# Kernel tuning notes

Measured on AMD Instinct MI355X. Metric: run time of the kernel, lower is better.

The kernel has to match this reference:

```python
import jax, jax.numpy as jnp
import numpy as np
from jax import lax

BAD = -10000.0
K = 10
W = 512  # window_size


def setup_inputs() -> dict:
    key = jax.random.key(0)
    k1, k2, k3, k4 = jax.random.split(key, 4)
    S, B, P, D, R = 4, 256, 32768, 256, 1000
    return {
        "relation": jax.random.randint(k1, (S, B), 0, R, dtype=jnp.int32),
        "head": jax.random.randint(k2, (S, B), 0, P, dtype=jnp.int32),
        "entity_embedding": jax.random.normal(k3, (S, P, D), dtype=jnp.float32),
        "relation_embedding": jax.random.normal(k4, (R, D), dtype=jnp.float32),
    }


def reference(relation, head, entity_embedding, relation_embedding):
    S, B = relation.shape
    P, D = entity_embedding.shape[1], entity_embedding.shape[2]
    Q = S * B            # total queries after all_gather
    NBEST = K + 1
    n_rep = -(-P // W)   # ceil

    # all_gather of queries across shards (every shard sees all queries)
    rel_all = relation.reshape(-1)                                   # (Q,)
    head_emb_all = entity_embedding[jnp.arange(S)[:, None], head]    # (S,B,D)
    head_emb_all = head_emb_all.reshape(Q, D)
    # DistMult score_tails: <h, r, t> ; fold h*r into one query vector
    qvec = head_emb_all * relation_embedding[rel_all]                # (Q,D)

    init_sc = jnp.full((S, Q, NBEST), BAD, dtype=jnp.float32)
    init_ix = jnp.full((S, Q, NBEST), P, dtype=jnp.int32)

    def step(carry, w):
        sc, ix = carry
        start = w * W
        # local idx of this window, clamped like the torch mask branch
        raw = start + jnp.arange(W, dtype=jnp.int32)                 # (W,)
        valid = raw < P
        slide = jnp.where(valid, raw, P - 1)
        neg = lax.dynamic_slice_in_dim(entity_embedding,
                                       jnp.minimum(start, P - W), W, axis=1)  # (S,W,D)
        scores_w = jnp.einsum('qd,swd->sqw', qvec, neg)              # (S,Q,W)
        scores_w = scores_w + BAD * (~valid).astype(scores_w.dtype)
        all_sc = jnp.concatenate([scores_w, sc], axis=-1)            # (S,Q,W+NBEST)
        all_ix = jnp.concatenate(
            [jnp.broadcast_to(slide, (S, Q, W)), ix], axis=-1)
        top_sc, top_pos = lax.top_k(all_sc, NBEST)
        top_ix = jnp.take_along_axis(all_ix, top_pos, axis=-1)
        return (top_sc, top_ix), None

    (best_sc, best_ix), _ = lax.scan(step, (init_sc, init_ix),
                                     jnp.arange(n_rep, dtype=jnp.int32))

    # all_to_all: (src_shard, dst_shard, bs, nbest) -> (dst, src, bs, nbest)
    best_sc = best_sc.reshape(S, S, B, NBEST).transpose(1, 0, 2, 3)
    best_ix = best_ix.reshape(S, S, B, NBEST).transpose(1, 0, 2, 3)

    # mask out placeholder / padding local indices (shard_counts == P)
    best_sc = best_sc + BAD * (best_ix >= P).astype(best_sc.dtype)

    # shard_and_idx_to_entity: interleaved global ids, padded column for idx==P
    base = jnp.arange(P, dtype=jnp.int32)[None, :] * S \
        + jnp.arange(S, dtype=jnp.int32)[:, None]                    # (S,P)
    table = jnp.concatenate(
        [base, jnp.full((S, 1), -1, dtype=jnp.int32)], axis=1)       # (S,P+1)
    src = jnp.arange(S, dtype=jnp.int32)[None, :, None, None]
    best_gid = table[src, best_ix]                                   # (S,S,B,NBEST)

    # per destination shard: merge the S per-source-shard top-(k+1) lists
    sc_flat = best_sc.transpose(0, 2, 1, 3).reshape(S, B, S * NBEST)
    gid_flat = best_gid.transpose(0, 2, 1, 3).reshape(S, B, S * NBEST)
    topk_sc, topk_pos = lax.top_k(sc_flat, K)                        # (S,B,K)
    topk_gid = jnp.take_along_axis(gid_flat, topk_pos, axis=-1)
    return topk_gid, topk_sc
```

## Files before the change

kernel.cpp:

```cpp
#include <hip/hip_runtime.h>

#define SS 4
#define BB 256
#define PP 32768
#define DD 256
#define QQ 1024
#define NN 131072
#define KTOP 10
#define QTILE 128
#define NCHUNK 64
#define CHROWS 2048
#define PANEL 64
#define NPANEL (CHROWS / PANEL)
#define JCH 8
#define MSLOT 20
#define ROWG 33
#define ROWE (ROWG * 8)
#define PANB (PANEL * ROWG * 16)
#define KEYMASK 0xFFFFF800u

typedef __attribute__((ext_vector_type(8))) short bf16x8;
typedef __attribute__((ext_vector_type(4))) float f32x4;
typedef __attribute__((ext_vector_type(4))) unsigned int u32x4;

static __device__ __forceinline__ short f2bf(float f) {
    union { float f; unsigned u; } v; v.f = f;
    unsigned r = (v.u + 0x7FFFu + ((v.u >> 16) & 1u)) >> 16;
    return (short)r;
}
static __device__ __forceinline__ bf16x8 cvt8(f32x4 a, f32x4 b) {
    bf16x8 r;
    r[0] = f2bf(a[0]); r[1] = f2bf(a[1]); r[2] = f2bf(a[2]); r[3] = f2bf(a[3]);
    r[4] = f2bf(b[0]); r[5] = f2bf(b[1]); r[6] = f2bf(b[2]); r[7] = f2bf(b[3]);
    return r;
}
static __device__ __forceinline__ unsigned umax(unsigned a, unsigned b) { return a > b ? a : b; }
static __device__ __forceinline__ unsigned umin(unsigned a, unsigned b) { return a < b ? a : b; }

__global__ void convert_e_kernel(const float* __restrict__ E, short* __restrict__ Ebf) {
    size_t i = ((size_t)blockIdx.x * 256 + threadIdx.x) * 8;
    f32x4 a = *(const f32x4*)(E + i);
    f32x4 b = *(const f32x4*)(E + i + 4);
    *(bf16x8*)(Ebf + i) = cvt8(a, b);
}

__global__ void qvec_kernel(const int* __restrict__ rel, const int* __restrict__ head,
                            const float* __restrict__ E, const float* __restrict__ R,
                            short* __restrict__ qbf) {
    int q = blockIdx.x, d = threadIdx.x;
    int s1 = q >> 8;
    float f = E[((size_t)(s1 * PP + head[q])) * DD + d] * R[(size_t)rel[q] * DD + d];
    qbf[q * DD + d] = f2bf(f);
}

__launch_bounds__(512, 4)
__global__ void score_topk_kernel(const short* __restrict__ Ebf, const short* __restrict__ qbf,
                                  unsigned* __restrict__ parts) {
    __shared__ __align__(16) char smem[2 * PANB];

    const int tid  = threadIdx.x;
    const int wave = tid >> 6;
    const int lane = tid & 63;
    const int quad = lane >> 4;
    const int mrow = lane & 15;
    const int mtile = blockIdx.x >> 6;
    const int chunk = blockIdx.x & 63;

    short* buf0 = (short*)smem;
    short* buf1 = (short*)(smem + PANB);

    bf16x8 afrag[8];
    {
        const int arow = mtile * QTILE + wave * 16 + mrow;
        #pragma unroll
        for (int ks = 0; ks < 8; ks++)
            afrag[ks] = *(const bf16x8*)(qbf + arow * DD + ks * 32 + quad * 8);
    }

    unsigned lst[4][4];
    #pragma unroll
    for (int r = 0; r < 4; r++)
        #pragma unroll
        for (int i = 0; i < 4; i++) lst[r][i] = 0u;

    const int n0c = chunk * CHROWS;

    bf16x8 st[4];
    #pragma unroll
    for (int it = 0; it < 4; it++) {
        int gi = it * 512 + tid, row = gi >> 5, slot = gi & 31;
        st[it] = *(const bf16x8*)(Ebf + (size_t)(n0c + row) * DD + slot * 8);
    }
    #pragma unroll
    for (int it = 0; it < 4; it++) {
        int gi = it * 512 + tid, row = gi >> 5, slot = gi & 31;
        *(bf16x8*)(buf0 + row * ROWE + slot * 8) = st[it];
    }

    int pc = mrow;

    for (int p = 0; p < NPANEL; p++) {
        short* bp = (p & 1) ? buf1 : buf0;
        short* bn = (p & 1) ? buf0 : buf1;
        __syncthreads();
        if (p + 1 < NPANEL) {
            const int n1 = n0c + (p + 1) * PANEL;
            #pragma unroll
            for (int it = 0; it < 4; it++) {
                int gi = it * 512 + tid, row = gi >> 5, slot = gi & 31;
                st[it] = *(const bf16x8*)(Ebf + (size_t)(n1 + row) * DD + slot * 8);
            }
        }

        f32x4 acc[4];
        #pragma unroll
        for (int nt = 0; nt < 4; nt++) acc[nt] = (f32x4){0.f, 0.f, 0.f, 0.f};
        #pragma unroll
        for (int ks = 0; ks < 8; ks++) {
            #pragma unroll
            for (int nt = 0; nt < 4; nt++) {
                int brow = nt * 16 + mrow;
                bf16x8 b = *(const bf16x8*)(bp + brow * ROWE + ks * 32 + quad * 8);
                acc[nt] = __builtin_amdgcn_mfma_f32_16x16x32_bf16(afrag[ks], b, acc[nt], 0, 0, 0);
            }
        }

        #pragma unroll
        for (int nt = 0; nt < 4; nt++) {
            const unsigned coln = (unsigned)(pc + nt * 16);
            #pragma unroll
            for (int r = 0; r < 4; r++) {
                unsigned enc = __float_as_uint(acc[nt][r] + 256.0f);
                unsigned key = (enc & KEYMASK) | coln;
                unsigned n0 = umin(umax(key, lst[r][0]), lst[r][1]);
                unsigned n1 = umin(umax(key, lst[r][1]), lst[r][2]);
                unsigned n2 = umin(umax(key, lst[r][2]), lst[r][3]);
                unsigned n3 = umax(key, lst[r][3]);
                lst[r][0] = n0; lst[r][1] = n1; lst[r][2] = n2; lst[r][3] = n3;
            }
        }
        pc += 64;

        if (p + 1 < NPANEL) {
            #pragma unroll
            for (int it = 0; it < 4; it++) {
                int gi = it * 512 + tid, row = gi >> 5, slot = gi & 31;
                *(bf16x8*)(bn + row * ROWE + slot * 8) = st[it];
            }
        }
    }

    unsigned* mw = (unsigned*)(smem + wave * 4096);
    #pragma unroll
    for (int r = 0; r < 4; r++) {
        u32x4 v; v[0] = lst[r][0]; v[1] = lst[r][1]; v[2] = lst[r][2]; v[3] = lst[r][3];
        *(u32x4*)(mw + (quad * 4 + r) * 64 + mrow * 4) = v;
    }
    if (lane < 16) {
        unsigned rr[JCH];
        #pragma unroll
        for (int i = 0; i < JCH; i++) rr[i] = 0u;
        #pragma unroll
        for (int j = 0; j < 16; j++) {
            u32x4 v = *(const u32x4*)(mw + lane * 64 + j * 4);
            #pragma unroll
            for (int e = 0; e < 4; e++) {
                unsigned x = v[e];
                unsigned t0 = umin(umax(x, rr[0]), rr[1]);
                unsigned t1 = umin(umax(x, rr[1]), rr[2]);
                unsigned t2 = umin(umax(x, rr[2]), rr[3]);
                unsigned t3 = umin(umax(x, rr[3]), rr[4]);
                unsigned t4 = umin(umax(x, rr[4]), rr[5]);
                unsigned t5 = umin(umax(x, rr[5]), rr[6]);
                unsigned t6 = umin(umax(x, rr[6]), rr[7]);
                unsigned t7 = umax(x, rr[7]);
                rr[0]=t0; rr[1]=t1; rr[2]=t2; rr[3]=t3; rr[4]=t4; rr[5]=t5; rr[6]=t6; rr[7]=t7;
            }
        }
        const int qg = mtile * QTILE + wave * 16 + lane;
        unsigned* dst = parts + ((size_t)qg * NCHUNK + chunk) * JCH;
        #pragma unroll
        for (int i = 0; i < JCH; i++) dst[i] = rr[JCH - 1 - i];
    }
}

__global__ void finalize_kernel(const int* __restrict__ rel, const int* __restrict__ head,
                                const float* __restrict__ E, const float* __restrict__ R,
                                const unsigned* __restrict__ parts, float* __restrict__ out) {
    __shared__ float qv[DD];
    __shared__ int   gl[MSLOT];
    __shared__ float rsc[MSLOT];
    __shared__ int   rgid[MSLOT];

    const int q = blockIdx.x;
    const int tid = threadIdx.x;
    const int wave = tid >> 6, lane = tid & 63;
    const int s1 = q >> 8;

    qv[tid] = E[((size_t)(s1 * PP + head[q])) * DD + tid] * R[(size_t)rel[q] * DD + tid];

    if (wave == 0) {
        unsigned run[JCH];
        const unsigned* src = parts + ((size_t)q * NCHUNK + lane) * JCH;
        #pragma unroll
        for (int j = 0; j < JCH; j++) run[j] = src[j];
        for (int r = 0; r < MSLOT; r++) {
            unsigned best = run[0]; int bl = lane;
            #pragma unroll
            for (int off = 32; off >= 1; off >>= 1) {
                unsigned ob = __shfl_xor(best, off);
                int ol = __shfl_xor(bl, off);
                if (ob > best || (ob == best && ol < bl)) { best = ob; bl = ol; }
            }
            if (lane == bl) {
                int col = (int)(best & 0x7FFu);
                int n = lane * CHROWS + col;
                gl[r] = ((n & (PP - 1)) << 2) | (n >> 15);
                #pragma unroll
                for (int j = 0; j < JCH - 1; j++) run[j] = run[j + 1];
                run[JCH - 1] = 0u;
            }
        }
    }
    __syncthreads();

    f32x4 qq = *(const f32x4*)(qv + lane * 4);
    #pragma unroll
    for (int c = 0; c < MSLOT / 4; c++) {
        int j = wave * (MSLOT / 4) + c;
        int gid = gl[j];
        int n = (gid & 3) * PP + (gid >> 2);
        f32x4 ev = *(const f32x4*)(E + (size_t)n * DD + lane * 4);
        f32x4 p = qq * ev;
        float s = (p[0] + p[1]) + (p[2] + p[3]);
        #pragma unroll
        for (int off = 32; off >= 1; off >>= 1) s += __shfl_xor(s, off);
        if (lane == 0) { rsc[j] = s; rgid[j] = gid; }
    }
    __syncthreads();

    if (tid < 64) {
        float a = (tid < MSLOT) ? rsc[tid] : -1e30f;
        int   g = (tid < MSLOT) ? rgid[tid] : 0;
        for (int r = 0; r < KTOP; r++) {
            float ps = a; int pg = g; int plm = tid;
            #pragma unroll
            for (int off = 32; off >= 1; off >>= 1) {
                float os = __shfl_xor(ps, off);
                int   og = __shfl_xor(pg, off);
                int   ol = __shfl_xor(plm, off);
                if (os > ps || (os == ps && ol < plm)) { ps = os; pg = og; plm = ol; }
            }
            if (tid == 0) {
                out[q * KTOP + r]             = (float)pg;
                out[QQ * KTOP + q * KTOP + r] = ps;
            }
            if (tid == plm) a = -1e30f;
        }
    }
}

extern "C" void kernel_launch(void* const* d_in, const int* in_sizes, int n_in,
                              void* d_out, int out_size, void* d_ws, size_t ws_size,
                              hipStream_t stream) {
    const int*   rel  = (const int*)d_in[0];
    const int*   head = (const int*)d_in[1];
    const float* E    = (const float*)d_in[2];
    const float* R    = (const float*)d_in[3];

    char* ws = (char*)d_ws;
    short* Ebf = (short*)ws;
    short* qbf = (short*)(ws + (size_t)NN * DD * 2);
    unsigned* parts = (unsigned*)(ws + (size_t)NN * DD * 2 + (size_t)QQ * DD * 2);

    convert_e_kernel<<<dim3(NN * DD / 8 / 256), dim3(256), 0, stream>>>(E, Ebf);
    qvec_kernel<<<dim3(QQ), dim3(DD), 0, stream>>>(rel, head, E, R, qbf);
    score_topk_kernel<<<dim3((QQ / QTILE) * NCHUNK), dim3(512), 0, stream>>>(Ebf, qbf, parts);
    finalize_kernel<<<dim3(QQ), dim3(256), 0, stream>>>(rel, head, E, R, parts, (float*)d_out);
}
```

Before: 320.8 us.

## Switch score kernel to 32x32x16 MFMA with 4 waves, fuse prep kernels

The score/top-k kernel now uses 32x32x16 bf16 MFMA tiles, with each of 4 waves handling 32 queries instead of 8 waves of 16 queries. This halves the LDS B-fragment reads per FLOP and changes the per-lane partial top-4 layout to 16 rows. The final per-wave merge is adjusted to match, using a padded stride and an added barrier. The E-to-bf16 conversion and qvec kernels are merged into one launch to save a launch. The trade-off is heavier register pressure (16x4 list entries plus 16 A fragments) and fewer waves per block, which may hurt latency hiding.

```diff
diff --git a/kernel.cpp b/kernel.cpp
--- a/kernel.cpp
+++ b/kernel.cpp
@@ -8,6 +8,7 @@
 #define NN 131072
 #define KTOP 10
 #define QTILE 128
+#define WQ 32
 #define NCHUNK 64
 #define CHROWS 2048
 #define PANEL 64
@@ -18,9 +19,11 @@
 #define ROWE (ROWG * 8)
 #define PANB (PANEL * ROWG * 16)
 #define KEYMASK 0xFFFFF800u
+#define MWS 132
 
 typedef __attribute__((ext_vector_type(8))) short bf16x8;
 typedef __attribute__((ext_vector_type(4))) float f32x4;
+typedef __attribute__((ext_vector_type(16))) float f32x16;
 typedef __attribute__((ext_vector_type(4))) unsigned int u32x4;
 
 static __device__ __forceinline__ short f2bf(float f) {
@@ -37,23 +40,23 @@
 static __device__ __forceinline__ unsigned umax(unsigned a, unsigned b) { return a > b ? a : b; }
 static __device__ __forceinline__ unsigned umin(unsigned a, unsigned b) { return a < b ? a : b; }
 
-__global__ void convert_e_kernel(const float* __restrict__ E, short* __restrict__ Ebf) {
-    size_t i = ((size_t)blockIdx.x * 256 + threadIdx.x) * 8;
-    f32x4 a = *(const f32x4*)(E + i);
-    f32x4 b = *(const f32x4*)(E + i + 4);
-    *(bf16x8*)(Ebf + i) = cvt8(a, b);
-}
-
-__global__ void qvec_kernel(const int* __restrict__ rel, const int* __restrict__ head,
+__global__ void prep_kernel(const int* __restrict__ rel, const int* __restrict__ head,
                             const float* __restrict__ E, const float* __restrict__ R,
-                            short* __restrict__ qbf) {
-    int q = blockIdx.x, d = threadIdx.x;
-    int s1 = q >> 8;
-    float f = E[((size_t)(s1 * PP + head[q])) * DD + d] * R[(size_t)rel[q] * DD + d];
-    qbf[q * DD + d] = f2bf(f);
-}
-
-__launch_bounds__(512, 4)
+                            short* __restrict__ Ebf, short* __restrict__ qbf) {
+    if (blockIdx.x < NN * DD / 8 / 256) {
+        size_t i = ((size_t)blockIdx.x * 256 + threadIdx.x) * 8;
+        f32x4 a = *(const f32x4*)(E + i);
+        f32x4 b = *(const f32x4*)(E + i + 4);
+        *(bf16x8*)(Ebf + i) = cvt8(a, b);
+    } else {
+        int q = blockIdx.x - NN * DD / 8 / 256, d = threadIdx.x;
+        int s1 = q >> 8;
+        float f = E[((size_t)(s1 * PP + head[q])) * DD + d] * R[(size_t)rel[q] * DD + d];
+        qbf[q * DD + d] = f2bf(f);
+    }
+}
+
+__launch_bounds__(256, 2)
 __global__ void score_topk_kernel(const short* __restrict__ Ebf, const short* __restrict__ qbf,
                                   unsigned* __restrict__ parts) {
     __shared__ __align__(16) char smem[2 * PANB];
@@ -61,43 +64,41 @@
     const int tid  = threadIdx.x;
     const int wave = tid >> 6;
     const int lane = tid & 63;
-    const int quad = lane >> 4;
-    const int mrow = lane & 15;
+    const int lh   = lane >> 5;
+    const int ln   = lane & 31;
     const int mtile = blockIdx.x >> 6;
     const int chunk = blockIdx.x & 63;
 
     short* buf0 = (short*)smem;
     short* buf1 = (short*)(smem + PANB);
 
-    bf16x8 afrag[8];
+    bf16x8 afrag[16];
     {
-        const int arow = mtile * QTILE + wave * 16 + mrow;
-        #pragma unroll
-        for (int ks = 0; ks < 8; ks++)
-            afrag[ks] = *(const bf16x8*)(qbf + arow * DD + ks * 32 + quad * 8);
-    }
-
-    unsigned lst[4][4];
-    #pragma unroll
-    for (int r = 0; r < 4; r++)
+        const int arow = mtile * QTILE + wave * WQ + ln;
+        #pragma unroll
+        for (int ks = 0; ks < 16; ks++)
+            afrag[ks] = *(const bf16x8*)(qbf + arow * DD + ks * 16 + lh * 8);
+    }
+
+    unsigned lst[16][4];
+    #pragma unroll
+    for (int r = 0; r < 16; r++)
         #pragma unroll
         for (int i = 0; i < 4; i++) lst[r][i] = 0u;
 
     const int n0c = chunk * CHROWS;
 
-    bf16x8 st[4];
-    #pragma unroll
-    for (int it = 0; it < 4; it++) {
-        int gi = it * 512 + tid, row = gi >> 5, slot = gi & 31;
+    bf16x8 st[8];
+    #pragma unroll
+    for (int it = 0; it < 8; it++) {
+        int gi = it * 256 + tid, row = gi >> 5, slot = gi & 31;
         st[it] = *(const bf16x8*)(Ebf + (size_t)(n0c + row) * DD + slot * 8);
     }
     #pragma unroll
-    for (int it = 0; it < 4; it++) {
-        int gi = it * 512 + tid, row = gi >> 5, slot = gi & 31;
+    for (int it = 0; it < 8; it++) {
+        int gi = it * 256 + tid, row = gi >> 5, slot = gi & 31;
         *(bf16x8*)(buf0 + row * ROWE + slot * 8) = st[it];
     }
-
-    int pc = mrow;
 
     for (int p = 0; p < NPANEL; p++) {
         short* bp = (p & 1) ? buf1 : buf0;
@@ -106,31 +107,25 @@
         if (p + 1 < NPANEL) {
             const int n1 = n0c + (p + 1) * PANEL;
             #pragma unroll
-            for (int it = 0; it < 4; it++) {
-                int gi = it * 512 + tid, row = gi >> 5, slot = gi & 31;
+            for (int it = 0; it < 8; it++) {
+                int gi = it * 256 + tid, row = gi >> 5, slot = gi & 31;
                 st[it] = *(const bf16x8*)(Ebf + (size_t)(n1 + row) * DD + slot * 8);
             }
         }
 
-        f32x4 acc[4];
-        #pragma unroll
-        for (int nt = 0; nt < 4; nt++) acc[nt] = (f32x4){0.f, 0.f, 0.f, 0.f};
-        #pragma unroll
-        for (int ks = 0; ks < 8; ks++) {
-            #pragma unroll
-            for (int nt = 0; nt < 4; nt++) {
-                int brow = nt * 16 + mrow;
-                bf16x8 b = *(const bf16x8*)(bp + brow * ROWE + ks * 32 + quad * 8);
-                acc[nt] = __builtin_amdgcn_mfma_f32_16x16x32_bf16(afrag[ks], b, acc[nt], 0, 0, 0);
-            }
-        }
-
-        #pragma unroll
-        for (int nt = 0; nt < 4; nt++) {
-            const unsigned coln = (unsigned)(pc + nt * 16);
-            #pragma unroll
-            for (int r = 0; r < 4; r++) {
-                unsigned enc = __float_as_uint(acc[nt][r] + 256.0f);
+        #pragma unroll
+        for (int ct = 0; ct < 2; ct++) {
+            f32x16 acc = {};
+            const short* bbase = bp + (ct * 32 + ln) * ROWE + lh * 8;
+            #pragma unroll
+            for (int ks = 0; ks < 16; ks++) {
+                bf16x8 b = *(const bf16x8*)(bbase + ks * 16);
+                acc = __builtin_amdgcn_mfma_f32_32x32x16_bf16(afrag[ks], b, acc, 0, 0, 0);
+            }
+            const unsigned coln = (unsigned)(p * 64 + ct * 32 + ln);
+            #pragma unroll
+            for (int r = 0; r < 16; r++) {
+                unsigned enc = __float_as_uint(acc[r] + 256.0f);
                 unsigned key = (enc & KEYMASK) | coln;
                 unsigned n0 = umin(umax(key, lst[r][0]), lst[r][1]);
                 unsigned n1 = umin(umax(key, lst[r][1]), lst[r][2]);
@@ -139,30 +134,31 @@
                 lst[r][0] = n0; lst[r][1] = n1; lst[r][2] = n2; lst[r][3] = n3;
             }
         }
-        pc += 64;
 
         if (p + 1 < NPANEL) {
             #pragma unroll
-            for (int it = 0; it < 4; it++) {
-                int gi = it * 512 + tid, row = gi >> 5, slot = gi & 31;
+            for (int it = 0; it < 8; it++) {
+                int gi = it * 256 + tid, row = gi >> 5, slot = gi & 31;
                 *(bf16x8*)(bn + row * ROWE + slot * 8) = st[it];
             }
         }
     }
 
-    unsigned* mw = (unsigned*)(smem + wave * 4096);
-    #pragma unroll
-    for (int r = 0; r < 4; r++) {
+    __syncthreads();
+    unsigned* mw = (unsigned*)smem + (size_t)wave * (WQ * MWS);
+    #pragma unroll
+    for (int r = 0; r < 16; r++) {
+        int q = (r & 3) + 8 * (r >> 2) + 4 * lh;
         u32x4 v; v[0] = lst[r][0]; v[1] = lst[r][1]; v[2] = lst[r][2]; v[3] = lst[r][3];
-        *(u32x4*)(mw + (quad * 4 + r) * 64 + mrow * 4) = v;
-    }
-    if (lane < 16) {
+        *(u32x4*)(mw + q * MWS + ln * 4) = v;
+    }
+    if (lane < 32) {
         unsigned rr[JCH];
         #pragma unroll
         for (int i = 0; i < JCH; i++) rr[i] = 0u;
         #pragma unroll
-        for (int j = 0; j < 16; j++) {
-            u32x4 v = *(const u32x4*)(mw + lane * 64 + j * 4);
+        for (int j = 0; j < 32; j++) {
+            u32x4 v = *(const u32x4*)(mw + lane * MWS + j * 4);
             #pragma unroll
             for (int e = 0; e < 4; e++) {
                 unsigned x = v[e];
@@ -177,7 +173,7 @@
                 rr[0]=t0; rr[1]=t1; rr[2]=t2; rr[3]=t3; rr[4]=t4; rr[5]=t5; rr[6]=t6; rr[7]=t7;
             }
         }
-        const int qg = mtile * QTILE + wave * 16 + lane;
+        const int qg = mtile * QTILE + wave * WQ + lane;
         unsigned* dst = parts + ((size_t)qg * NCHUNK + chunk) * JCH;
         #pragma unroll
         for (int i = 0; i < JCH; i++) dst[i] = rr[JCH - 1 - i];
@@ -273,8 +269,7 @@
     short* qbf = (short*)(ws + (size_t)NN * DD * 2);
     unsigned* parts = (unsigned*)(ws + (size_t)NN * DD * 2 + (size_t)QQ * DD * 2);
 
-    convert_e_kernel<<<dim3(NN * DD / 8 / 256), dim3(256), 0, stream>>>(E, Ebf);
-    qvec_kernel<<<dim3(QQ), dim3(DD), 0, stream>>>(rel, head, E, R, qbf);
-    score_topk_kernel<<<dim3((QQ / QTILE) * NCHUNK), dim3(512), 0, stream>>>(Ebf, qbf, parts);
+    prep_kernel<<<dim3(NN * DD / 8 / 256 + QQ), dim3(256), 0, stream>>>(rel, head, E, R, Ebf, qbf);
+    score_topk_kernel<<<dim3((QQ / QTILE) * NCHUNK), dim3(256), 0, stream>>>(Ebf, qbf, parts);
     finalize_kernel<<<dim3(QQ), dim3(256), 0, stream>>>(rel, head, E, R, parts, (float*)d_out);
 }
```

Result: faster. 309.7 us (-3.4%).
